# Kernel tuning notes

Measured on AMD Instinct MI355X. Metric: run time of the kernel, lower is better.

## Reference

```python
import jax, jax.numpy as jnp
import numpy as np

B, TQ, TS, E, D = 8, 100, 100, 512, 512

def setup_inputs() -> dict:
    key = jax.random.key(0)
    k1, k2, k3, k4, k5 = jax.random.split(key, 5)
    src_reps = jax.random.normal(k1, (B, TQ, TS, E), dtype=jnp.float32)
    tgt_reps = jax.random.normal(k2, (B, TQ, TS, E), dtype=jnp.float32)
    mask = jnp.ones((B, TQ, TS), dtype=jnp.float32)
    # attn_1: Linear(2E -> D) with bias; attn_2: Linear(D -> 1) no bias
    W1 = jax.random.normal(k3, (2 * E, D), dtype=jnp.float32) / np.sqrt(2 * E)
    b1 = jax.random.normal(k4, (D,), dtype=jnp.float32) * 0.01
    w2 = jax.random.normal(k5, (D,), dtype=jnp.float32) / np.sqrt(D)
    return {"src_reps": src_reps, "tgt_reps": tgt_reps, "mask": mask,
            "W1": W1, "b1": b1, "w2": w2}

def reference(src_reps, tgt_reps, mask, W1, b1, w2):
    # cat over feature dim: [B,TQ,TS,2E]
    cat_reps = jnp.concatenate([src_reps, tgt_reps], axis=-1)
    # two small linears + tanh -> scores [B,TQ,TS]
    h = jnp.tanh(jnp.einsum('bqse,ed->bqsd', cat_reps, W1) + b1)
    attn_scores = jnp.einsum('bqsd,d->bqs', h, w2)
    attn_scores = mask * attn_scores  # multiplicative mask (as in source)
    attn_weights = jax.nn.softmax(attn_scores, axis=2)
    # weighted sum over src dim -> [B,TQ,E]
    attn_out = jnp.einsum('bqs,bqse->bqe', attn_weights, src_reps)
    return (attn_out, attn_weights)
```

## Files before the change

### kernel.cpp

```cpp
#include <hip/hip_runtime.h>
#include <hip/hip_bf16.h>

#define B_   8
#define TQ_  100
#define TS_  100
#define E_   512
#define D_   512
#define K_   1024
#define M_   (B_*TQ_*TS_)

#define MT   64
#define BK   64
#define NTHREADS 512

typedef __attribute__((ext_vector_type(4))) float f32x4;
typedef __attribute__((ext_vector_type(8))) short bf16x8;

__device__ __forceinline__ short f2bf(float f) {
  __hip_bfloat16 h = __float2bfloat16(f);
  return *reinterpret_cast<short*>(&h);
}

__device__ __forceinline__ float fast_tanh(float x) {
  float e = __expf(2.0f * x);
  return 1.0f - 2.0f / (e + 1.0f);
}

__global__ void prep_w1(const float* __restrict__ W1, short* __restrict__ W1t) {
  int idx = blockIdx.x * 256 + threadIdx.x;
  int k = idx >> 9;
  int n = idx & (D_ - 1);
  W1t[(size_t)n * K_ + k] = f2bf(W1[idx]);
}

__launch_bounds__(NTHREADS, 4)
__global__ void scores_kernel(const float* __restrict__ src,
                              const float* __restrict__ tgt,
                              const short* __restrict__ W1t,
                              const float* __restrict__ b1,
                              const float* __restrict__ w2,
                              float* __restrict__ scores) {
  __shared__ __align__(16) char Alds[MT * 128];
  __shared__ __align__(16) char Blds[D_ * 128];
  __shared__ float s_sc[MT];

  const int tid  = threadIdx.x;
  const int wave = tid >> 6;
  const int lane = tid & 63;
  const int lr   = lane & 15;
  const int lg   = lane >> 4;
  const int m0   = blockIdx.x * MT;

  f32x4 acc[4][4];
  #pragma unroll
  for (int i = 0; i < 4; i++)
    #pragma unroll
    for (int j = 0; j < 4; j++)
      acc[i][j] = (f32x4){0.f, 0.f, 0.f, 0.f};

  const int ar = tid >> 3;
  const int ac = (tid & 7) * 8;

  for (int k0 = 0; k0 < K_; k0 += BK) {
    {
      const float* Ap = ((k0 < E_) ? src : tgt)
                        + (size_t)(m0 + ar) * E_ + (k0 & (E_ - 1)) + ac;
      f32x4 v0 = *reinterpret_cast<const f32x4*>(Ap);
      f32x4 v1 = *reinterpret_cast<const f32x4*>(Ap + 4);
      bf16x8 w;
      w[0] = f2bf(v0[0]); w[1] = f2bf(v0[1]); w[2] = f2bf(v0[2]); w[3] = f2bf(v0[3]);
      w[4] = f2bf(v1[0]); w[5] = f2bf(v1[1]); w[6] = f2bf(v1[2]); w[7] = f2bf(v1[3]);
      *reinterpret_cast<bf16x8*>(Alds + ar * 128 + ((ac * 2) ^ ((ar & 7) << 4))) = w;
    }
    #pragma unroll
    for (int i = 0; i < 8; i++) {
      int n = ar + i * 64;
      bf16x8 v = *reinterpret_cast<const bf16x8*>(W1t + (size_t)n * K_ + k0 + ac);
      *reinterpret_cast<bf16x8*>(Blds + n * 128 + ((ac * 2) ^ ((n & 7) << 4))) = v;
    }
    __syncthreads();

    #pragma unroll
    for (int kk = 0; kk < 2; kk++) {
      const int kb = kk * 64 + lg * 16;
      bf16x8 a[4], b[4];
      #pragma unroll
      for (int mi = 0; mi < 4; mi++) {
        int row = mi * 16 + lr;
        a[mi] = *reinterpret_cast<const bf16x8*>(
                    Alds + row * 128 + (kb ^ ((row & 7) << 4)));
      }
      #pragma unroll
      for (int ni = 0; ni < 4; ni++) {
        int n = wave * 64 + ni * 16 + lr;
        b[ni] = *reinterpret_cast<const bf16x8*>(
                    Blds + n * 128 + (kb ^ ((n & 7) << 4)));
      }
      #pragma unroll
      for (int mi = 0; mi < 4; mi++)
        #pragma unroll
        for (int ni = 0; ni < 4; ni++)
          acc[mi][ni] = __builtin_amdgcn_mfma_f32_16x16x32_bf16(
                            a[mi], b[ni], acc[mi][ni], 0, 0, 0);
    }
    __syncthreads();
  }

  if (tid < MT) s_sc[tid] = 0.0f;
  __syncthreads();

  float b1v[4], w2v[4];
  #pragma unroll
  for (int ni = 0; ni < 4; ni++) {
    int n = wave * 64 + ni * 16 + lr;
    b1v[ni] = b1[n];
    w2v[ni] = w2[n];
  }
  #pragma unroll
  for (int mi = 0; mi < 4; mi++) {
    #pragma unroll
    for (int r = 0; r < 4; r++) {
      float p = 0.0f;
      #pragma unroll
      for (int ni = 0; ni < 4; ni++)
        p += fast_tanh(acc[mi][ni][r] + b1v[ni]) * w2v[ni];
      p += __shfl_xor(p, 1);
      p += __shfl_xor(p, 2);
      p += __shfl_xor(p, 4);
      p += __shfl_xor(p, 8);
      if (lr == 0) atomicAdd(&s_sc[mi * 16 + lg * 4 + r], p);
    }
  }
  __syncthreads();
  if (tid < MT) scores[m0 + tid] = s_sc[tid];
}

__global__ void softmax_wsum(const float* __restrict__ src,
                             const float* __restrict__ mask,
                             const float* __restrict__ scores,
                             float* __restrict__ out) {
  const int row = blockIdx.x;
  const int tid = threadIdx.x;
  __shared__ float s_e[TS_];

  float v = 0.0f;
  if (tid < TS_) {
    v = scores[row * TS_ + tid] * mask[row * TS_ + tid];
    s_e[tid] = v;
  }
  __syncthreads();
  float mx = -3.0e38f;
  for (int s = 0; s < TS_; s++) mx = fmaxf(mx, s_e[s]);
  __syncthreads();
  if (tid < TS_) s_e[tid] = __expf(v - mx);
  __syncthreads();
  float sum = 0.0f;
  for (int s = 0; s < TS_; s++) sum += s_e[s];
  const float inv = 1.0f / sum;

  float* out_attn = out;
  float* out_w    = out + (size_t)B_ * TQ_ * E_;
  if (tid < TS_) out_w[row * TS_ + tid] = s_e[tid] * inv;

  const float* sp = src + (size_t)row * TS_ * E_ + tid;
  float acc = 0.0f;
  #pragma unroll 4
  for (int s = 0; s < TS_; s++) acc = fmaf(s_e[s], sp[(size_t)s * E_], acc);
  out_attn[row * E_ + tid] = acc * inv;
}

extern "C" void kernel_launch(void* const* d_in, const int* in_sizes, int n_in,
                              void* d_out, int out_size, void* d_ws, size_t ws_size,
                              hipStream_t stream) {
  const float* src  = (const float*)d_in[0];
  const float* tgt  = (const float*)d_in[1];
  const float* mask = (const float*)d_in[2];
  const float* W1   = (const float*)d_in[3];
  const float* b1   = (const float*)d_in[4];
  const float* w2   = (const float*)d_in[5];

  short* W1t    = (short*)d_ws;
  float* scores = (float*)((char*)d_ws + (size_t)D_ * K_ * 2);

  float* out = (float*)d_out;

  hipLaunchKernelGGL(prep_w1, dim3((K_ * D_) / 256), dim3(256), 0, stream, W1, W1t);
  hipLaunchKernelGGL(scores_kernel, dim3(M_ / MT), dim3(NTHREADS), 0, stream,
                     src, tgt, W1t, b1, w2, scores);
  hipLaunchKernelGGL(softmax_wsum, dim3(B_ * TQ_), dim3(512), 0, stream,
                     src, mask, scores, out);
}
```

Measured before the change: 161.3 us.

## Retile scores GEMM to 128x256 with double-buffered async LDS loads for W1

Changes the scores GEMM tile from 64 rows by all 512 columns to 128 rows by 256 columns, splitting N across two blocks that write partial scores summed later in the softmax kernel. W1 is pre-swizzled on the host-side prep kernel so it can be streamed directly into LDS via global_load_lds into a double buffer, while the next A tile is prefetched into registers during the MFMA loop. The aim is to overlap global loads with compute and shrink per-block LDS, at the cost of reading each A tile twice and an extra sync per iteration.

```diff
diff --git a/kernel.cpp b/kernel.cpp
--- a/kernel.cpp
+++ b/kernel.cpp
@@ -9,7 +9,8 @@
 #define K_   1024
 #define M_   (B_*TQ_*TS_)
 
-#define MT   64
+#define MT   128
+#define NT   256
 #define BK   64
 #define NTHREADS 512
 
@@ -26,30 +27,42 @@
   return 1.0f - 2.0f / (e + 1.0f);
 }
 
-__global__ void prep_w1(const float* __restrict__ W1, short* __restrict__ W1t) {
+__device__ __forceinline__ void gld16(const void* g, void* l) {
+  __builtin_amdgcn_global_load_lds(
+      (const __attribute__((address_space(1))) unsigned int*)g,
+      (__attribute__((address_space(3))) unsigned int*)l, 16, 0, 0);
+}
+
+__global__ void prep_w1(const float* __restrict__ W1, short* __restrict__ W1sw) {
   int idx = blockIdx.x * 256 + threadIdx.x;
   int k = idx >> 9;
   int n = idx & (D_ - 1);
-  W1t[(size_t)n * K_ + k] = f2bf(W1[idx]);
+  int byte = (k * 2) ^ ((n & 7) << 4);
+  W1sw[(size_t)n * K_ + (byte >> 1)] = f2bf(W1[idx]);
 }
 
 __launch_bounds__(NTHREADS, 4)
 __global__ void scores_kernel(const float* __restrict__ src,
                               const float* __restrict__ tgt,
-                              const short* __restrict__ W1t,
+                              const short* __restrict__ W1sw,
                               const float* __restrict__ b1,
                               const float* __restrict__ w2,
-                              float* __restrict__ scores) {
+                              float* __restrict__ sc0,
+                              float* __restrict__ sc1) {
   __shared__ __align__(16) char Alds[MT * 128];
-  __shared__ __align__(16) char Blds[D_ * 128];
-  __shared__ float s_sc[MT];
+  __shared__ __align__(16) char Blds[2][NT * 128];
 
   const int tid  = threadIdx.x;
   const int wave = tid >> 6;
   const int lane = tid & 63;
   const int lr   = lane & 15;
   const int lg   = lane >> 4;
-  const int m0   = blockIdx.x * MT;
+  const int wr   = wave >> 2;
+  const int wc   = wave & 3;
+  const int bm   = blockIdx.x >> 1;
+  const int bn   = blockIdx.x & 1;
+  const int m0   = bm * MT;
+  const int n0   = bn * NT;
 
   f32x4 acc[4][4];
   #pragma unroll
@@ -58,43 +71,70 @@
     for (int j = 0; j < 4; j++)
       acc[i][j] = (f32x4){0.f, 0.f, 0.f, 0.f};
 
-  const int ar = tid >> 3;
-  const int ac = (tid & 7) * 8;
-
-  for (int k0 = 0; k0 < K_; k0 += BK) {
-    {
-      const float* Ap = ((k0 < E_) ? src : tgt)
-                        + (size_t)(m0 + ar) * E_ + (k0 & (E_ - 1)) + ac;
-      f32x4 v0 = *reinterpret_cast<const f32x4*>(Ap);
-      f32x4 v1 = *reinterpret_cast<const f32x4*>(Ap + 4);
-      bf16x8 w;
-      w[0] = f2bf(v0[0]); w[1] = f2bf(v0[1]); w[2] = f2bf(v0[2]); w[3] = f2bf(v0[3]);
-      w[4] = f2bf(v1[0]); w[5] = f2bf(v1[1]); w[6] = f2bf(v1[2]); w[7] = f2bf(v1[3]);
-      *reinterpret_cast<bf16x8*>(Alds + ar * 128 + ((ac * 2) ^ ((ar & 7) << 4))) = w;
-    }
-    #pragma unroll
-    for (int i = 0; i < 8; i++) {
-      int n = ar + i * 64;
-      bf16x8 v = *reinterpret_cast<const bf16x8*>(W1t + (size_t)n * K_ + k0 + ac);
-      *reinterpret_cast<bf16x8*>(Blds + n * 128 + ((ac * 2) ^ ((n & 7) << 4))) = v;
-    }
-    __syncthreads();
-
+  const int ra = tid >> 2;
+  const int ka = (tid & 3) * 16;
+  const int swA = (ra & 7) << 4;
+  const int bl_row = lane >> 3;
+  const int bl_in  = (lane & 7) * 16;
+
+  #pragma unroll
+  for (int j = 0; j < 4; j++) {
+    int nl = wave * 32 + j * 8 + bl_row;
+    const char* gp = (const char*)W1sw + (size_t)(n0 + nl) * 2048 + bl_in;
+    gld16(gp, Blds[0] + wave * 4096 + j * 1024);
+  }
+  {
+    const float* Ap = src + (size_t)(m0 + ra) * E_ + ka;
+    f32x4 r0 = *reinterpret_cast<const f32x4*>(Ap);
+    f32x4 r1 = *reinterpret_cast<const f32x4*>(Ap + 4);
+    f32x4 r2 = *reinterpret_cast<const f32x4*>(Ap + 8);
+    f32x4 r3 = *reinterpret_cast<const f32x4*>(Ap + 12);
+    bf16x8 w0, w1;
+    w0[0]=f2bf(r0[0]); w0[1]=f2bf(r0[1]); w0[2]=f2bf(r0[2]); w0[3]=f2bf(r0[3]);
+    w0[4]=f2bf(r1[0]); w0[5]=f2bf(r1[1]); w0[6]=f2bf(r1[2]); w0[7]=f2bf(r1[3]);
+    w1[0]=f2bf(r2[0]); w1[1]=f2bf(r2[1]); w1[2]=f2bf(r2[2]); w1[3]=f2bf(r2[3]);
+    w1[4]=f2bf(r3[0]); w1[5]=f2bf(r3[1]); w1[6]=f2bf(r3[2]); w1[7]=f2bf(r3[3]);
+    int kb = ka * 2;
+    *reinterpret_cast<bf16x8*>(Alds + ra * 128 + ( kb       ^ swA)) = w0;
+    *reinterpret_cast<bf16x8*>(Alds + ra * 128 + ((kb + 16) ^ swA)) = w1;
+  }
+  __syncthreads();
+
+  int cur = 0;
+  for (int t = 0; t < 16; ++t) {
+    const int k0n = (t + 1) * BK;
+    const bool pf = (t < 15);
+    f32x4 r0, r1, r2, r3;
+    if (pf) {
+      const float* Ap = ((k0n < E_) ? src : tgt)
+                        + (size_t)(m0 + ra) * E_ + (k0n & (E_ - 1)) + ka;
+      r0 = *reinterpret_cast<const f32x4*>(Ap);
+      r1 = *reinterpret_cast<const f32x4*>(Ap + 4);
+      r2 = *reinterpret_cast<const f32x4*>(Ap + 8);
+      r3 = *reinterpret_cast<const f32x4*>(Ap + 12);
+      #pragma unroll
+      for (int j = 0; j < 4; j++) {
+        int nl = wave * 32 + j * 8 + bl_row;
+        const char* gp = (const char*)W1sw + (size_t)(n0 + nl) * 2048
+                         + (size_t)k0n * 2 + bl_in;
+        gld16(gp, Blds[cur ^ 1] + wave * 4096 + j * 1024);
+      }
+    }
     #pragma unroll
     for (int kk = 0; kk < 2; kk++) {
       const int kb = kk * 64 + lg * 16;
       bf16x8 a[4], b[4];
       #pragma unroll
       for (int mi = 0; mi < 4; mi++) {
-        int row = mi * 16 + lr;
+        int row = wr * 64 + mi * 16 + lr;
         a[mi] = *reinterpret_cast<const bf16x8*>(
                     Alds + row * 128 + (kb ^ ((row & 7) << 4)));
       }
       #pragma unroll
       for (int ni = 0; ni < 4; ni++) {
-        int n = wave * 64 + ni * 16 + lr;
+        int nr = wc * 64 + ni * 16 + lr;
         b[ni] = *reinterpret_cast<const bf16x8*>(
-                    Blds + n * 128 + (kb ^ ((n & 7) << 4)));
+                    Blds[cur] + nr * 128 + (kb ^ ((nr & 7) << 4)));
       }
       #pragma unroll
       for (int mi = 0; mi < 4; mi++)
@@ -104,15 +144,28 @@
                             a[mi], b[ni], acc[mi][ni], 0, 0, 0);
     }
     __syncthreads();
-  }
-
+    if (pf) {
+      bf16x8 w0, w1;
+      w0[0]=f2bf(r0[0]); w0[1]=f2bf(r0[1]); w0[2]=f2bf(r0[2]); w0[3]=f2bf(r0[3]);
+      w0[4]=f2bf(r1[0]); w0[5]=f2bf(r1[1]); w0[6]=f2bf(r1[2]); w0[7]=f2bf(r1[3]);
+      w1[0]=f2bf(r2[0]); w1[1]=f2bf(r2[1]); w1[2]=f2bf(r2[2]); w1[3]=f2bf(r2[3]);
+      w1[4]=f2bf(r3[0]); w1[5]=f2bf(r3[1]); w1[6]=f2bf(r3[2]); w1[7]=f2bf(r3[3]);
+      int kb = ka * 2;
+      *reinterpret_cast<bf16x8*>(Alds + ra * 128 + ( kb       ^ swA)) = w0;
+      *reinterpret_cast<bf16x8*>(Alds + ra * 128 + ((kb + 16) ^ swA)) = w1;
+    }
+    __syncthreads();
+    cur ^= 1;
+  }
+
+  float* s_sc = (float*)Alds;
   if (tid < MT) s_sc[tid] = 0.0f;
   __syncthreads();
 
   float b1v[4], w2v[4];
   #pragma unroll
   for (int ni = 0; ni < 4; ni++) {
-    int n = wave * 64 + ni * 16 + lr;
+    int n = n0 + wc * 64 + ni * 16 + lr;
     b1v[ni] = b1[n];
     w2v[ni] = w2[n];
   }
@@ -128,16 +181,20 @@
       p += __shfl_xor(p, 2);
       p += __shfl_xor(p, 4);
       p += __shfl_xor(p, 8);
-      if (lr == 0) atomicAdd(&s_sc[mi * 16 + lg * 4 + r], p);
-    }
-  }
-  __syncthreads();
-  if (tid < MT) scores[m0 + tid] = s_sc[tid];
+      if (lr == 0) atomicAdd(&s_sc[wr * 64 + mi * 16 + lg * 4 + r], p);
+    }
+  }
+  __syncthreads();
+  if (tid < MT) {
+    float* scp = bn ? sc1 : sc0;
+    scp[m0 + tid] = s_sc[tid];
+  }
 }
 
 __global__ void softmax_wsum(const float* __restrict__ src,
                              const float* __restrict__ mask,
-                             const float* __restrict__ scores,
+                             const float* __restrict__ sc0,
+                             const float* __restrict__ sc1,
                              float* __restrict__ out) {
   const int row = blockIdx.x;
   const int tid = threadIdx.x;
@@ -145,7 +202,7 @@
 
   float v = 0.0f;
   if (tid < TS_) {
-    v = scores[row * TS_ + tid] * mask[row * TS_ + tid];
+    v = (sc0[row * TS_ + tid] + sc1[row * TS_ + tid]) * mask[row * TS_ + tid];
     s_e[tid] = v;
   }
   __syncthreads();
@@ -179,14 +236,15 @@
   const float* b1   = (const float*)d_in[4];
   const float* w2   = (const float*)d_in[5];
 
-  short* W1t    = (short*)d_ws;
-  float* scores = (float*)((char*)d_ws + (size_t)D_ * K_ * 2);
+  short* W1sw = (short*)d_ws;
+  float* sc0  = (float*)((char*)d_ws + (size_t)D_ * K_ * 2);
+  float* sc1  = sc0 + M_;
 
   float* out = (float*)d_out;
 
-  hipLaunchKernelGGL(prep_w1, dim3((K_ * D_) / 256), dim3(256), 0, stream, W1, W1t);
-  hipLaunchKernelGGL(scores_kernel, dim3(M_ / MT), dim3(NTHREADS), 0, stream,
-                     src, tgt, W1t, b1, w2, scores);
+  hipLaunchKernelGGL(prep_w1, dim3((K_ * D_) / 256), dim3(256), 0, stream, W1, W1sw);
+  hipLaunchKernelGGL(scores_kernel, dim3((M_ / MT) * 2), dim3(NTHREADS), 0, stream,
+                     src, tgt, W1sw, b1, w2, sc0, sc1);
   hipLaunchKernelGGL(softmax_wsum, dim3(B_ * TQ_), dim3(512), 0, stream,
-                     src, mask, scores, out);
-}
+                     src, mask, sc0, sc1, out);
+}
```

After: 175.3 us. +8.6%, slower.

## Double-buffer GEMM tiles, load W1 via direct global-to-LDS, enlarge M tile

Applied to the files above, without the earlier changes.

The scores GEMM now double-buffers A and B tiles in LDS, prefetching the next K slice while MFMAs run on the current one. Pre-swizzled bf16 W1 is loaded straight into LDS with global_load_lds instead of passing through registers. The M tile grows from 64 to 128 rows with a 2x4 wave grid, which halves how often W1 is reloaded per output row, and MFMA priority is raised during compute. The cost is about 160KB of LDS and more accumulators, so occupancy drops to about one block per CU.

```diff
diff --git a/kernel.cpp b/kernel.cpp
--- a/kernel.cpp
+++ b/kernel.cpp
@@ -9,7 +9,8 @@
 #define K_   1024
 #define M_   (B_*TQ_*TS_)
 
-#define MT   64
+#define MT   128
+#define NT   512
 #define BK   64
 #define NTHREADS 512
 
@@ -26,93 +27,142 @@
   return 1.0f - 2.0f / (e + 1.0f);
 }
 
-__global__ void prep_w1(const float* __restrict__ W1, short* __restrict__ W1t) {
+__device__ __forceinline__ void gld16(const void* g, void* l) {
+  __builtin_amdgcn_global_load_lds(
+      (const __attribute__((address_space(1))) unsigned int*)g,
+      (__attribute__((address_space(3))) unsigned int*)l, 16, 0, 0);
+}
+
+__global__ void prep_w1(const float* __restrict__ W1, short* __restrict__ W1sw) {
   int idx = blockIdx.x * 256 + threadIdx.x;
   int k = idx >> 9;
   int n = idx & (D_ - 1);
-  W1t[(size_t)n * K_ + k] = f2bf(W1[idx]);
-}
-
-__launch_bounds__(NTHREADS, 4)
+  int byte = (k * 2) ^ ((n & 7) << 4);
+  W1sw[(size_t)n * K_ + (byte >> 1)] = f2bf(W1[idx]);
+}
+
+__launch_bounds__(NTHREADS, 2)
 __global__ void scores_kernel(const float* __restrict__ src,
                               const float* __restrict__ tgt,
-                              const short* __restrict__ W1t,
+                              const short* __restrict__ W1sw,
                               const float* __restrict__ b1,
                               const float* __restrict__ w2,
                               float* __restrict__ scores) {
-  __shared__ __align__(16) char Alds[MT * 128];
-  __shared__ __align__(16) char Blds[D_ * 128];
-  __shared__ float s_sc[MT];
+  __shared__ __align__(16) char Alds[2][MT * 128];
+  __shared__ __align__(16) char Blds[2][NT * 128];
 
   const int tid  = threadIdx.x;
   const int wave = tid >> 6;
   const int lane = tid & 63;
   const int lr   = lane & 15;
   const int lg   = lane >> 4;
+  const int wr   = wave >> 2;
+  const int wc   = wave & 3;
   const int m0   = blockIdx.x * MT;
 
-  f32x4 acc[4][4];
+  f32x4 acc[4][8];
   #pragma unroll
   for (int i = 0; i < 4; i++)
     #pragma unroll
-    for (int j = 0; j < 4; j++)
+    for (int j = 0; j < 8; j++)
       acc[i][j] = (f32x4){0.f, 0.f, 0.f, 0.f};
 
-  const int ar = tid >> 3;
-  const int ac = (tid & 7) * 8;
-
-  for (int k0 = 0; k0 < K_; k0 += BK) {
-    {
-      const float* Ap = ((k0 < E_) ? src : tgt)
-                        + (size_t)(m0 + ar) * E_ + (k0 & (E_ - 1)) + ac;
-      f32x4 v0 = *reinterpret_cast<const f32x4*>(Ap);
-      f32x4 v1 = *reinterpret_cast<const f32x4*>(Ap + 4);
-      bf16x8 w;
-      w[0] = f2bf(v0[0]); w[1] = f2bf(v0[1]); w[2] = f2bf(v0[2]); w[3] = f2bf(v0[3]);
-      w[4] = f2bf(v1[0]); w[5] = f2bf(v1[1]); w[6] = f2bf(v1[2]); w[7] = f2bf(v1[3]);
-      *reinterpret_cast<bf16x8*>(Alds + ar * 128 + ((ac * 2) ^ ((ar & 7) << 4))) = w;
-    }
-    #pragma unroll
-    for (int i = 0; i < 8; i++) {
-      int n = ar + i * 64;
-      bf16x8 v = *reinterpret_cast<const bf16x8*>(W1t + (size_t)n * K_ + k0 + ac);
-      *reinterpret_cast<bf16x8*>(Blds + n * 128 + ((ac * 2) ^ ((n & 7) << 4))) = v;
-    }
+  const int ra  = tid >> 2;
+  const int ka  = (tid & 3) * 16;
+  const int swA = (ra & 7) << 4;
+  const int br = tid >> 3;
+  const int bb = (tid & 7) * 16;
+
+  #define ISSUE_A(R0,R1,R2,R3,K0)                                              \
+    {                                                                          \
+      const float* Ap = (((K0) < E_) ? src : tgt)                              \
+                        + (size_t)(m0 + ra) * E_ + ((K0) & (E_ - 1)) + ka;     \
+      R0 = *reinterpret_cast<const f32x4*>(Ap);                                \
+      R1 = *reinterpret_cast<const f32x4*>(Ap + 4);                            \
+      R2 = *reinterpret_cast<const f32x4*>(Ap + 8);                            \
+      R3 = *reinterpret_cast<const f32x4*>(Ap + 12);                           \
+    }
+
+  #define WRITE_A(R0,R1,R2,R3,BUF)                                             \
+    {                                                                          \
+      bf16x8 w0, w1;                                                           \
+      w0[0]=f2bf(R0[0]); w0[1]=f2bf(R0[1]); w0[2]=f2bf(R0[2]); w0[3]=f2bf(R0[3]);\
+      w0[4]=f2bf(R1[0]); w0[5]=f2bf(R1[1]); w0[6]=f2bf(R1[2]); w0[7]=f2bf(R1[3]);\
+      w1[0]=f2bf(R2[0]); w1[1]=f2bf(R2[1]); w1[2]=f2bf(R2[2]); w1[3]=f2bf(R2[3]);\
+      w1[4]=f2bf(R3[0]); w1[5]=f2bf(R3[1]); w1[6]=f2bf(R3[2]); w1[7]=f2bf(R3[3]);\
+      int kb = ka * 2;                                                         \
+      *reinterpret_cast<bf16x8*>((BUF) + ra * 128 + ( kb       ^ swA)) = w0;   \
+      *reinterpret_cast<bf16x8*>((BUF) + ra * 128 + ((kb + 16) ^ swA)) = w1;   \
+    }
+
+  #define ISSUE_B(K0,BUF)                                                      \
+    {                                                                          \
+      _Pragma("unroll")                                                        \
+      for (int j = 0; j < 8; j++) {                                            \
+        const char* gp = (const char*)W1sw + (size_t)(j * 64 + br) * 2048      \
+                         + (size_t)(K0) * 2 + bb;                              \
+        gld16(gp, (BUF) + j * 8192 + tid * 16);                                \
+      }                                                                        \
+    }
+
+  #define MFMA_PHASE(KK,AB,BB2)                                                \
+    {                                                                          \
+      const int kb = (KK) * 64 + lg * 16;                                      \
+      bf16x8 a[4], b[8];                                                       \
+      _Pragma("unroll")                                                        \
+      for (int mi = 0; mi < 4; mi++) {                                         \
+        int row = wr * 64 + mi * 16 + lr;                                      \
+        a[mi] = *reinterpret_cast<const bf16x8*>(                              \
+                    (AB) + row * 128 + (kb ^ ((row & 7) << 4)));               \
+      }                                                                        \
+      _Pragma("unroll")                                                        \
+      for (int ni = 0; ni < 8; ni++) {                                         \
+        int nr = wc * 128 + ni * 16 + lr;                                      \
+        b[ni] = *reinterpret_cast<const bf16x8*>(                              \
+                    (BB2) + nr * 128 + (kb ^ ((nr & 7) << 4)));                \
+      }                                                                        \
+      __builtin_amdgcn_s_setprio(1);                                           \
+      _Pragma("unroll")                                                        \
+      for (int mi = 0; mi < 4; mi++)                                           \
+        _Pragma("unroll")                                                      \
+        for (int ni = 0; ni < 8; ni++)                                         \
+          acc[mi][ni] = __builtin_amdgcn_mfma_f32_16x16x32_bf16(               \
+                            a[mi], b[ni], acc[mi][ni], 0, 0, 0);               \
+      __builtin_amdgcn_s_setprio(0);                                           \
+    }
+
+  {
+    f32x4 r0, r1, r2, r3;
+    ISSUE_A(r0, r1, r2, r3, 0);
+    ISSUE_B(0, Blds[0]);
+    WRITE_A(r0, r1, r2, r3, Alds[0]);
+  }
+  __syncthreads();
+
+  for (int t = 0; t < 16; ++t) {
+    const int cur = t & 1;
+    const int nxt = cur ^ 1;
+    const bool pf = (t < 15);
+    const int k0n = (t + 1) * BK;
+    f32x4 r0, r1, r2, r3;
+    if (pf) ISSUE_A(r0, r1, r2, r3, k0n);
+    MFMA_PHASE(0, Alds[cur], Blds[cur]);
+    if (pf) {
+      ISSUE_B(k0n, Blds[nxt]);
+      WRITE_A(r0, r1, r2, r3, Alds[nxt]);
+    }
+    MFMA_PHASE(1, Alds[cur], Blds[cur]);
     __syncthreads();
-
-    #pragma unroll
-    for (int kk = 0; kk < 2; kk++) {
-      const int kb = kk * 64 + lg * 16;
-      bf16x8 a[4], b[4];
-      #pragma unroll
-      for (int mi = 0; mi < 4; mi++) {
-        int row = mi * 16 + lr;
-        a[mi] = *reinterpret_cast<const bf16x8*>(
-                    Alds + row * 128 + (kb ^ ((row & 7) << 4)));
-      }
-      #pragma unroll
-      for (int ni = 0; ni < 4; ni++) {
-        int n = wave * 64 + ni * 16 + lr;
-        b[ni] = *reinterpret_cast<const bf16x8*>(
-                    Blds + n * 128 + (kb ^ ((n & 7) << 4)));
-      }
-      #pragma unroll
-      for (int mi = 0; mi < 4; mi++)
-        #pragma unroll
-        for (int ni = 0; ni < 4; ni++)
-          acc[mi][ni] = __builtin_amdgcn_mfma_f32_16x16x32_bf16(
-                            a[mi], b[ni], acc[mi][ni], 0, 0, 0);
-    }
-    __syncthreads();
-  }
-
+  }
+
+  float* s_sc = (float*)Alds;
   if (tid < MT) s_sc[tid] = 0.0f;
   __syncthreads();
 
-  float b1v[4], w2v[4];
+  float b1v[8], w2v[8];
   #pragma unroll
-  for (int ni = 0; ni < 4; ni++) {
-    int n = wave * 64 + ni * 16 + lr;
+  for (int ni = 0; ni < 8; ni++) {
+    int n = wc * 128 + ni * 16 + lr;
     b1v[ni] = b1[n];
     w2v[ni] = w2[n];
   }
@@ -122,13 +172,13 @@
     for (int r = 0; r < 4; r++) {
       float p = 0.0f;
       #pragma unroll
-      for (int ni = 0; ni < 4; ni++)
+      for (int ni = 0; ni < 8; ni++)
         p += fast_tanh(acc[mi][ni][r] + b1v[ni]) * w2v[ni];
       p += __shfl_xor(p, 1);
       p += __shfl_xor(p, 2);
       p += __shfl_xor(p, 4);
       p += __shfl_xor(p, 8);
-      if (lr == 0) atomicAdd(&s_sc[mi * 16 + lg * 4 + r], p);
+      if (lr == 0) atomicAdd(&s_sc[wr * 64 + mi * 16 + lg * 4 + r], p);
     }
   }
   __syncthreads();
@@ -179,14 +229,14 @@
   const float* b1   = (const float*)d_in[4];
   const float* w2   = (const float*)d_in[5];
 
-  short* W1t    = (short*)d_ws;
+  short* W1sw   = (short*)d_ws;
   float* scores = (float*)((char*)d_ws + (size_t)D_ * K_ * 2);
 
   float* out = (float*)d_out;
 
-  hipLaunchKernelGGL(prep_w1, dim3((K_ * D_) / 256), dim3(256), 0, stream, W1, W1t);
+  hipLaunchKernelGGL(prep_w1, dim3((K_ * D_) / 256), dim3(256), 0, stream, W1, W1sw);
   hipLaunchKernelGGL(scores_kernel, dim3(M_ / MT), dim3(NTHREADS), 0, stream,
-                     src, tgt, W1t, b1, w2, scores);
+                     src, tgt, W1sw, b1, w2, scores);
   hipLaunchKernelGGL(softmax_wsum, dim3(B_ * TQ_), dim3(512), 0, stream,
                      src, mask, scores, out);
 }
```

After: 187.2 us. 1.16x slower.

## Software-pipeline scores GEMM with async global-to-LDS W1 loads and multi-buffering

Applied to the files above, without the earlier changes.

Replaces the load-sync-compute loop with a software pipeline over 32-wide K chunks. W1 is pre-swizzled into chunk-contiguous bf16 tiles and streamed straight into double-buffered LDS with global_load_lds. Activations are prefetched two chunks ahead in registers and staged in a triple-buffered A tile. Each iteration ends with one barrier plus explicit waitcnt, and MFMA priority is raised, so memory latency overlaps the matrix work. In exchange the code relies on hand-placed waitcnt and sched barriers and hard-coded chunk counts, which are fragile to get right.

```diff
diff --git a/kernel.cpp b/kernel.cpp
--- a/kernel.cpp
+++ b/kernel.cpp
@@ -10,11 +10,12 @@
 #define M_   (B_*TQ_*TS_)
 
 #define MT   64
-#define BK   64
+#define NCH  32
 #define NTHREADS 512
 
 typedef __attribute__((ext_vector_type(4))) float f32x4;
 typedef __attribute__((ext_vector_type(8))) short bf16x8;
+typedef __attribute__((ext_vector_type(4))) short bf16x4;
 
 __device__ __forceinline__ short f2bf(float f) {
   __hip_bfloat16 h = __float2bfloat16(f);
@@ -26,23 +27,38 @@
   return 1.0f - 2.0f / (e + 1.0f);
 }
 
-__global__ void prep_w1(const float* __restrict__ W1, short* __restrict__ W1t) {
+__device__ __forceinline__ void gld16(const void* g, void* l) {
+  __builtin_amdgcn_global_load_lds(
+      (const __attribute__((address_space(1))) unsigned int*)g,
+      (__attribute__((address_space(3))) unsigned int*)l, 16, 0, 0);
+}
+
+__device__ __forceinline__ bf16x4 packA(f32x4 v) {
+  bf16x4 o;
+  o[0] = f2bf(v[0]); o[1] = f2bf(v[1]); o[2] = f2bf(v[2]); o[3] = f2bf(v[3]);
+  return o;
+}
+
+__global__ void prep_w1(const float* __restrict__ W1, short* __restrict__ W1sw2) {
   int idx = blockIdx.x * 256 + threadIdx.x;
   int k = idx >> 9;
   int n = idx & (D_ - 1);
-  W1t[(size_t)n * K_ + k] = f2bf(W1[idx]);
+  int c = k >> 5;
+  int o = (k >> 3) & 3;
+  int w = k & 7;
+  int slot = o ^ (n & 3);
+  W1sw2[((size_t)c << 14) + (size_t)((n * 4 + slot) << 3) + w] = f2bf(W1[idx]);
 }
 
 __launch_bounds__(NTHREADS, 4)
 __global__ void scores_kernel(const float* __restrict__ src,
                               const float* __restrict__ tgt,
-                              const short* __restrict__ W1t,
+                              const short* __restrict__ W1sw2,
                               const float* __restrict__ b1,
                               const float* __restrict__ w2,
                               float* __restrict__ scores) {
-  __shared__ __align__(16) char Alds[MT * 128];
-  __shared__ __align__(16) char Blds[D_ * 128];
-  __shared__ float s_sc[MT];
+  __shared__ __align__(16) char Alds[3][MT * 64];
+  __shared__ __align__(16) char Blds[2][D_ * 64];
 
   const int tid  = threadIdx.x;
   const int wave = tid >> 6;
@@ -50,6 +66,12 @@
   const int lr   = lane & 15;
   const int lg   = lane >> 4;
   const int m0   = blockIdx.x * MT;
+  const int boff = (lg * 16) ^ ((lr & 3) << 4);
+
+  const int ra    = tid >> 3;
+  const int kaf   = (tid & 7) * 4;
+  const int awoff = ra * 64 + (((tid & 7) * 8) ^ ((ra & 3) << 4));
+  const size_t rowoff = (size_t)(m0 + ra) * E_;
 
   f32x4 acc[4][4];
   #pragma unroll
@@ -58,54 +80,78 @@
     for (int j = 0; j < 4; j++)
       acc[i][j] = (f32x4){0.f, 0.f, 0.f, 0.f};
 
-  const int ar = tid >> 3;
-  const int ac = (tid & 7) * 8;
-
-  for (int k0 = 0; k0 < K_; k0 += BK) {
-    {
-      const float* Ap = ((k0 < E_) ? src : tgt)
-                        + (size_t)(m0 + ar) * E_ + (k0 & (E_ - 1)) + ac;
-      f32x4 v0 = *reinterpret_cast<const f32x4*>(Ap);
-      f32x4 v1 = *reinterpret_cast<const f32x4*>(Ap + 4);
-      bf16x8 w;
-      w[0] = f2bf(v0[0]); w[1] = f2bf(v0[1]); w[2] = f2bf(v0[2]); w[3] = f2bf(v0[3]);
-      w[4] = f2bf(v1[0]); w[5] = f2bf(v1[1]); w[6] = f2bf(v1[2]); w[7] = f2bf(v1[3]);
-      *reinterpret_cast<bf16x8*>(Alds + ar * 128 + ((ac * 2) ^ ((ar & 7) << 4))) = w;
+  #define APTR(T) ((const f32x4*)((((T) < 16) ? src : tgt) + rowoff + (((T) * 32) & 511) + kaf))
+
+  #define ISSUE_B(CC, BUF)                                                     \
+    { const char* gb = (const char*)W1sw2 + ((size_t)(CC) << 15) + tid * 16;   \
+      _Pragma("unroll")                                                        \
+      for (int j = 0; j < 4; j++)                                              \
+        gld16(gb + j * 8192, (BUF) + j * 8192 + wave * 1024); }
+
+  #define COMPUTE(AR, BBUF)                                                    \
+    { bf16x8 a[4], b[4];                                                       \
+      _Pragma("unroll")                                                        \
+      for (int mi = 0; mi < 4; mi++)                                           \
+        a[mi] = *(const bf16x8*)(Alds[AR] + (mi * 16 + lr) * 64 + boff);       \
+      _Pragma("unroll")                                                        \
+      for (int ni = 0; ni < 4; ni++)                                           \
+        b[ni] = *(const bf16x8*)((BBUF) + (wave * 64 + ni * 16 + lr) * 64 + boff); \
+      __builtin_amdgcn_s_setprio(1);                                           \
+      _Pragma("unroll")                                                        \
+      for (int mi = 0; mi < 4; mi++)                                           \
+        _Pragma("unroll")                                                      \
+        for (int ni = 0; ni < 4; ni++)                                         \
+          acc[mi][ni] = __builtin_amdgcn_mfma_f32_16x16x32_bf16(               \
+                            a[mi], b[ni], acc[mi][ni], 0, 0, 0);               \
+      __builtin_amdgcn_s_setprio(0); }
+
+  #define BODY(AR, AW, BR, RW, RI, CC)                                         \
+    {                                                                          \
+      *(bf16x4*)(Alds[AW] + awoff) = packA(RW);                                \
+      ISSUE_B((CC) + 1, Blds[(BR) ^ 1]);                                       \
+      __builtin_amdgcn_sched_barrier(0);                                       \
+      RI = *APTR((CC) + 2);                                                    \
+      COMPUTE(AR, Blds[BR]);                                                   \
+      asm volatile("s_waitcnt vmcnt(1) lgkmcnt(0)" ::: "memory");              \
+      __builtin_amdgcn_sched_barrier(0);                                       \
+      __builtin_amdgcn_s_barrier();                                            \
+      __builtin_amdgcn_sched_barrier(0);                                       \
     }
-    #pragma unroll
-    for (int i = 0; i < 8; i++) {
-      int n = ar + i * 64;
-      bf16x8 v = *reinterpret_cast<const bf16x8*>(W1t + (size_t)n * K_ + k0 + ac);
-      *reinterpret_cast<bf16x8*>(Blds + n * 128 + ((ac * 2) ^ ((n & 7) << 4))) = v;
-    }
-    __syncthreads();
-
-    #pragma unroll
-    for (int kk = 0; kk < 2; kk++) {
-      const int kb = kk * 64 + lg * 16;
-      bf16x8 a[4], b[4];
-      #pragma unroll
-      for (int mi = 0; mi < 4; mi++) {
-        int row = mi * 16 + lr;
-        a[mi] = *reinterpret_cast<const bf16x8*>(
-                    Alds + row * 128 + (kb ^ ((row & 7) << 4)));
-      }
-      #pragma unroll
-      for (int ni = 0; ni < 4; ni++) {
-        int n = wave * 64 + ni * 16 + lr;
-        b[ni] = *reinterpret_cast<const bf16x8*>(
-                    Blds + n * 128 + (kb ^ ((n & 7) << 4)));
-      }
-      #pragma unroll
-      for (int mi = 0; mi < 4; mi++)
-        #pragma unroll
-        for (int ni = 0; ni < 4; ni++)
-          acc[mi][ni] = __builtin_amdgcn_mfma_f32_16x16x32_bf16(
-                            a[mi], b[ni], acc[mi][ni], 0, 0, 0);
-    }
-    __syncthreads();
-  }
-
+
+  f32x4 r0, r1;
+  ISSUE_B(0, Blds[0]);
+  __builtin_amdgcn_sched_barrier(0);
+  r0 = *APTR(0);
+  r1 = *APTR(1);
+  *(bf16x4*)(Alds[0] + awoff) = packA(r0);
+  asm volatile("s_waitcnt vmcnt(1) lgkmcnt(0)" ::: "memory");
+  __builtin_amdgcn_sched_barrier(0);
+  __builtin_amdgcn_s_barrier();
+  __builtin_amdgcn_sched_barrier(0);
+
+  for (int i = 0; i < 5; ++i) {
+    const int c = 6 * i;
+    BODY(0, 1, 0, r1, r0, c + 0);
+    BODY(1, 2, 1, r0, r1, c + 1);
+    BODY(2, 0, 0, r1, r0, c + 2);
+    BODY(0, 1, 1, r0, r1, c + 3);
+    BODY(1, 2, 0, r1, r0, c + 4);
+    BODY(2, 0, 1, r0, r1, c + 5);
+  }
+
+  {
+    *(bf16x4*)(Alds[1] + awoff) = packA(r1);
+    ISSUE_B(31, Blds[1]);
+    COMPUTE(0, Blds[0]);
+    asm volatile("s_waitcnt vmcnt(0) lgkmcnt(0)" ::: "memory");
+    __builtin_amdgcn_sched_barrier(0);
+    __builtin_amdgcn_s_barrier();
+    __builtin_amdgcn_sched_barrier(0);
+    COMPUTE(1, Blds[1]);
+  }
+
+  float* s_sc = (float*)Blds[0];
+  __builtin_amdgcn_s_barrier();
   if (tid < MT) s_sc[tid] = 0.0f;
   __syncthreads();
 
@@ -179,14 +225,14 @@
   const float* b1   = (const float*)d_in[4];
   const float* w2   = (const float*)d_in[5];
 
-  short* W1t    = (short*)d_ws;
+  short* W1sw2  = (short*)d_ws;
   float* scores = (float*)((char*)d_ws + (size_t)D_ * K_ * 2);
 
   float* out = (float*)d_out;
 
-  hipLaunchKernelGGL(prep_w1, dim3((K_ * D_) / 256), dim3(256), 0, stream, W1, W1t);
+  hipLaunchKernelGGL(prep_w1, dim3((K_ * D_) / 256), dim3(256), 0, stream, W1, W1sw2);
   hipLaunchKernelGGL(scores_kernel, dim3(M_ / MT), dim3(NTHREADS), 0, stream,
-                     src, tgt, W1t, b1, w2, scores);
+                     src, tgt, W1sw2, b1, w2, scores);
   hipLaunchKernelGGL(softmax_wsum, dim3(B_ * TQ_), dim3(512), 0, stream,
                      src, mask, scores, out);
 }
```

New measurement: 180.4 us. +11.8%, slower.
